# Performance work log

Measured on AMD Instinct MI355X. Metric: run time of the kernel, lower is better.

Reference implementation:

```python
import jax, jax.numpy as jnp
import numpy as np

B, L, D_IN, D_OUT = 8, 2048, 256, 256


def setup_inputs() -> dict:
    key = jax.random.key(0)
    ks = jax.random.split(key, 7)
    s_in = 1.0 / np.sqrt(D_IN)
    return {
        "x": jax.random.normal(ks[0], (B, L, D_IN), dtype=jnp.float32),
        "Wq": jax.random.uniform(ks[1], (D_OUT, D_IN), jnp.float32, -s_in, s_in),
        "bq": jax.random.uniform(ks[2], (D_OUT,), jnp.float32, -s_in, s_in),
        "Wk": jax.random.uniform(ks[3], (D_OUT, D_IN), jnp.float32, -s_in, s_in),
        "bk": jax.random.uniform(ks[4], (D_OUT,), jnp.float32, -s_in, s_in),
        "Wv": jax.random.uniform(ks[5], (D_OUT, D_IN), jnp.float32, -s_in, s_in),
        "bv": jax.random.uniform(ks[6], (D_OUT,), jnp.float32, -s_in, s_in),
    }


def reference(x, Wq, bq, Wk, bk, Wv, bv):
    # QKV projections (torch Linear: y = x @ W.T + b)
    Q = jnp.einsum("bld,od->blo", x, Wq) + bq  # [B, L, D_OUT]
    K = jnp.einsum("bld,od->blo", x, Wk) + bk
    V = jnp.einsum("bld,od->blo", x, Wv) + bv
    scale = jnp.float32(D_OUT) ** 0.5
    E = jnp.einsum("bqd,bkd->bqk", Q, K) / scale  # [B, L, L]
    # NON-STANDARD: softmax over dim=1 (the query axis / columns of E)
    A = jax.nn.softmax(E, axis=1)
    C = jnp.einsum("bqk,bkd->bqd", A, V)  # [B, L, D_OUT]
    S_p = jnp.concatenate([Q, C], axis=1)  # [B, 2L, D_OUT]
    return (S_p, A)
```

## Files before the change

### kernel.cpp

```cpp
#include <hip/hip_runtime.h>
#include <hip/hip_bf16.h>
#include <stdint.h>

#define B_ 8
#define L_ 2048
#define D_ 256

typedef unsigned short u16;
typedef __attribute__((ext_vector_type(4))) float f32x4;
typedef __attribute__((ext_vector_type(8))) short bf16x8;

__device__ __forceinline__ u16 f2b(float f) {
  union { float f; unsigned u; } v; v.f = f;
  unsigned r = v.u + 0x7FFFu + ((v.u >> 16) & 1u);
  return (u16)(r >> 16);
}

__device__ __forceinline__ float b2f(u16 h) {
  union { unsigned u; float f; } v; v.u = (unsigned)h << 16; return v.f;
}

__device__ __forceinline__ void comb(float& m, float& s, float m2, float s2) {
  float mn = fmaxf(m, m2);
  s = s * __expf(m - mn) + s2 * __expf(m2 - mn);
  m = mn;
}

__device__ __forceinline__ void async_copy16(const void* g, u16* l) {
  __builtin_amdgcn_global_load_lds(
      (const __attribute__((address_space(1))) unsigned*)g,
      (__attribute__((address_space(3))) unsigned*)l,
      16, 0, 0);
}

template<int KD>
__device__ __forceinline__ void gemm_core_db(const u16* __restrict__ Ag,
                                             const u16* __restrict__ Bg,
                                             int tile_m, int tile_n,
                                             u16* lds, f32x4 acc[4][4]) {
  const int tid  = threadIdx.x;
  const int wave = tid >> 6, lane = tid & 63;
  const int qd = lane >> 4, ln = lane & 15;
  const int wm = wave >> 1, wn = wave & 1;
  const int lrow = lane >> 2;
  const int lcol = (lane & 3) * 8;
  const u16* Abase = Ag + (size_t)tile_m * KD + lcol;
  const u16* Bbase = Bg + (size_t)tile_n * KD + lcol;
  constexpr int NT = KD / 32;

#pragma unroll
  for (int j = 0; j < 2; ++j) {
    const int r0 = j * 64 + wave * 16;
    async_copy16(Abase + (size_t)(r0 + lrow) * KD, lds + r0 * 32);
    async_copy16(Bbase + (size_t)(r0 + lrow) * KD, lds + 4096 + r0 * 32);
  }

#pragma unroll
  for (int t = 0; t < NT; ++t) {
    asm volatile("s_waitcnt vmcnt(0)" ::: "memory");
    __builtin_amdgcn_s_barrier();
    __builtin_amdgcn_sched_barrier(0);
    const int cur = (t & 1) * 8192;
    if (t + 1 < NT) {
      const int nxt = ((t + 1) & 1) * 8192;
      const int k0 = (t + 1) * 32;
#pragma unroll
      for (int j = 0; j < 2; ++j) {
        const int r0 = j * 64 + wave * 16;
        async_copy16(Abase + (size_t)(r0 + lrow) * KD + k0, lds + nxt + r0 * 32);
        async_copy16(Bbase + (size_t)(r0 + lrow) * KD + k0, lds + nxt + 4096 + r0 * 32);
      }
      __builtin_amdgcn_sched_barrier(0);
    }
    bf16x8 af[4], bg[4];
#pragma unroll
    for (int i = 0; i < 4; ++i) {
      af[i] = *(const bf16x8*)(lds + cur + (wm * 64 + i * 16 + ln) * 32 + qd * 8);
      bg[i] = *(const bf16x8*)(lds + cur + 4096 + (wn * 64 + i * 16 + ln) * 32 + qd * 8);
    }
#pragma unroll
    for (int i = 0; i < 4; ++i)
#pragma unroll
      for (int j = 0; j < 4; ++j)
        acc[i][j] = __builtin_amdgcn_mfma_f32_16x16x32_bf16(af[i], bg[j], acc[i][j], 0, 0, 0);
  }
}

__global__ __launch_bounds__(256) void cvt_kernel(const float* __restrict__ x,
    const float* __restrict__ Wq, const float* __restrict__ Wk, const float* __restrict__ Wv,
    u16* __restrict__ xb, u16* __restrict__ Wb) {
  const int i = blockIdx.x * 256 + threadIdx.x;
  const int NX4 = (B_ * L_ * D_) / 4;
  f32x4 v;
  u16* dst;
  if (i < NX4) {
    v = ((const f32x4*)x)[i];
    dst = xb + (size_t)i * 4;
  } else {
    int wi = i - NX4;
    int z = wi >> 14;
    int off = wi & 16383;
    const float* W = (z == 0) ? Wq : (z == 1 ? Wk : Wv);
    v = ((const f32x4*)W)[off];
    dst = Wb + (size_t)z * 65536 + (size_t)off * 4;
  }
  unsigned p0 = (unsigned)f2b(v.x) | ((unsigned)f2b(v.y) << 16);
  unsigned p1 = (unsigned)f2b(v.z) | ((unsigned)f2b(v.w) << 16);
  *(uint2*)dst = make_uint2(p0, p1);
}

__global__ __launch_bounds__(256) void qkv_gemm(const u16* __restrict__ xb, const u16* __restrict__ Wb,
    const float* __restrict__ bq, const float* __restrict__ bk, const float* __restrict__ bv,
    u16* __restrict__ Qb, u16* __restrict__ Kb, u16* __restrict__ Vbt,
    float* __restrict__ out_sp) {
  __shared__ u16 lds[16384];
  const int z = blockIdx.z;
  const float* bias = (z == 0) ? bq : (z == 1 ? bk : bv);
  const int tile_m = blockIdx.x * 128, tile_n = blockIdx.y * 128;
  f32x4 acc[4][4];
#pragma unroll
  for (int i = 0; i < 4; ++i)
#pragma unroll
    for (int j = 0; j < 4; ++j) acc[i][j] = (f32x4){0.f, 0.f, 0.f, 0.f};
  gemm_core_db<256>(xb, Wb + (size_t)z * 256 * 256, tile_m, tile_n, lds, acc);

  const int tid = threadIdx.x, lane = tid & 63, wave = tid >> 6;
  const int qd = lane >> 4, ln = lane & 15, wm = wave >> 1, wn = wave & 1;

  if (z < 2) {
    u16* dst = (z == 0) ? Qb : Kb;
#pragma unroll
    for (int p = 0; p < 2; ++p) {
      __syncthreads();
      if (wm == p) {
#pragma unroll
        for (int i = 0; i < 4; ++i)
#pragma unroll
          for (int j = 0; j < 4; ++j) {
            const int col = wn * 64 + j * 16 + ln;
            const float bvv = bias[tile_n + col];
#pragma unroll
            for (int r = 0; r < 4; ++r) {
              const int row = i * 16 + qd * 4 + r;
              const float val = acc[i][j][r] + bvv;
              lds[row * 128 + col] = f2b(val);
              if (z == 0) {
                const int grow = tile_m + p * 64 + row;
                const int bb = grow >> 11, l = grow & 2047;
                out_sp[((size_t)bb * (2 * L_) + l) * D_ + tile_n + col] = val;
              }
            }
          }
      }
      __syncthreads();
      const int r = tid >> 2;
#pragma unroll
      for (int s = 0; s < 4; ++s) {
        const int chunk = (tid & 3) + s * 4;
        bf16x8 v = *(const bf16x8*)(lds + r * 128 + chunk * 8);
        *(bf16x8*)(dst + (size_t)(tile_m + p * 64 + r) * D_ + tile_n + chunk * 8) = v;
      }
    }
  } else {
    const int bb = tile_m >> 11, l0 = tile_m & 2047;
    u16* dstb = Vbt + (size_t)bb * D_ * L_;
#pragma unroll
    for (int p = 0; p < 2; ++p) {
      __syncthreads();
      if (wn == p) {
#pragma unroll
        for (int i = 0; i < 4; ++i)
#pragma unroll
          for (int j = 0; j < 4; ++j) {
            const int col = j * 16 + ln;
            const float bvv = bias[tile_n + p * 64 + col];
#pragma unroll
            for (int r = 0; r < 4; ++r) {
              const int row = wm * 64 + i * 16 + qd * 4 + r;
              lds[col * 128 + row] = f2b(acc[i][j][r] + bvv);
            }
          }
      }
      __syncthreads();
      const int dr = tid >> 2;
#pragma unroll
      for (int s = 0; s < 4; ++s) {
        const int chunk = (tid & 3) + s * 4;
        bf16x8 v = *(const bf16x8*)(lds + dr * 128 + chunk * 8);
        *(bf16x8*)(dstb + (size_t)(tile_n + p * 64 + dr) * L_ + l0 + chunk * 8) = v;
      }
    }
  }
}

__global__ __launch_bounds__(256) void e_gemm(const u16* __restrict__ Qb, const u16* __restrict__ Kb,
                                              u16* __restrict__ Eb16,
                                              float* __restrict__ pm, float* __restrict__ ps) {
  __shared__ u16 lds[16384];
  __shared__ float sm_m[4][64], sm_s[4][64];
  const int b = blockIdx.z;
  const int tile_m = blockIdx.x * 128, tile_n = blockIdx.y * 128;
  f32x4 acc[4][4];
#pragma unroll
  for (int i = 0; i < 4; ++i)
#pragma unroll
    for (int j = 0; j < 4; ++j) acc[i][j] = (f32x4){0.f, 0.f, 0.f, 0.f};
  gemm_core_db<256>(Qb + (size_t)b * L_ * D_, Kb + (size_t)b * L_ * D_, tile_m, tile_n, lds, acc);

  u16* Eb = Eb16 + (size_t)b * L_ * L_;
  const int tid = threadIdx.x;
  const int lane = tid & 63, wave = tid >> 6;
  const int qd = lane >> 4, ln = lane & 15, wm = wave >> 1, wn = wave & 1;

#pragma unroll
  for (int j = 0; j < 4; ++j) {
    float m = -1e30f;
#pragma unroll
    for (int i = 0; i < 4; ++i)
#pragma unroll
      for (int r = 0; r < 4; ++r)
        m = fmaxf(m, acc[i][j][r] * 0.0625f);
    float s = 0.f;
#pragma unroll
    for (int i = 0; i < 4; ++i)
#pragma unroll
      for (int r = 0; r < 4; ++r)
        s += __expf(acc[i][j][r] * 0.0625f - m);
    comb(m, s, __shfl_xor(m, 16), __shfl_xor(s, 16));
    comb(m, s, __shfl_xor(m, 32), __shfl_xor(s, 32));
    if (qd == 0) { sm_m[wave][j * 16 + ln] = m; sm_s[wave][j * 16 + ln] = s; }
  }
  __syncthreads();
  if (tid < 128) {
    const int w = tid >> 6, c = tid & 63;
    float m = sm_m[w][c], s = sm_s[w][c];
    comb(m, s, sm_m[w + 2][c], sm_s[w + 2][c]);
    const size_t idx = (size_t)blockIdx.x * (B_ * L_) + (size_t)b * L_ + tile_n + w * 64 + c;
    pm[idx] = m;
    ps[idx] = s;
  }

#pragma unroll
  for (int p = 0; p < 2; ++p) {
    __syncthreads();
    if (wm == p) {
#pragma unroll
      for (int i = 0; i < 4; ++i)
#pragma unroll
        for (int j = 0; j < 4; ++j) {
          const int col = wn * 64 + j * 16 + ln;
#pragma unroll
          for (int r = 0; r < 4; ++r) {
            const int row = i * 16 + qd * 4 + r;
            lds[row * 128 + col] = f2b(acc[i][j][r] * 0.0625f);
          }
        }
    }
    __syncthreads();
    const int r = tid >> 2;
#pragma unroll
    for (int s = 0; s < 4; ++s) {
      const int chunk = (tid & 3) + s * 4;
      bf16x8 v = *(const bf16x8*)(lds + r * 128 + chunk * 8);
      *(bf16x8*)(Eb + (size_t)(tile_m + p * 64 + r) * L_ + tile_n + chunk * 8) = v;
    }
  }
}

__global__ __launch_bounds__(256) void stats_reduce(const float* __restrict__ pm,
                                                    const float* __restrict__ ps,
                                                    float* __restrict__ mOut, float* __restrict__ rOut) {
  const int idx = blockIdx.x * 256 + threadIdx.x;
  float m = -1e30f, s = 0.f;
#pragma unroll
  for (int t = 0; t < 16; ++t)
    comb(m, s, pm[t * (B_ * L_) + idx], ps[t * (B_ * L_) + idx]);
  mOut[idx] = m;
  rOut[idx] = 1.0f / s;
}

__global__ __launch_bounds__(256) void av_fused(const u16* __restrict__ Eb16, const u16* __restrict__ Vbt,
                                                const float* __restrict__ mArr, const float* __restrict__ rArr,
                                                float* __restrict__ Aout, float* __restrict__ out_sp) {
  __shared__ __align__(16) u16 lds_b[2][2][256 * 32];
  __shared__ __align__(16) u16 lds_a[2][2][32 * 32];
  const int b = blockIdx.x;
  const int tile_m = blockIdx.y * 32;
  const int tid = threadIdx.x;
  const int wave = tid >> 6, lane = tid & 63;
  const int qd = lane >> 4, ln = lane & 15;
  const int lrow = lane >> 2, lcol = (lane & 3) * 8;

  const u16* Vb_ = Vbt + (size_t)b * D_ * L_ + lcol;
  const int arow = tid >> 3, koff = (tid & 7) * 8;
  const int aks = koff >> 5, acol = koff & 31;
  const u16* Erow = Eb16 + ((size_t)b * L_ + tile_m + arow) * L_ + koff;
  float* Arow = Aout + ((size_t)b * L_ + tile_m + arow) * L_ + koff;
  const float* mrow = mArr + (size_t)b * L_ + koff;
  const float* rrow = rArr + (size_t)b * L_ + koff;

  f32x4 acc[2][4];
#pragma unroll
  for (int i = 0; i < 2; ++i)
#pragma unroll
    for (int j = 0; j < 4; ++j) acc[i][j] = (f32x4){0.f, 0.f, 0.f, 0.f};

#pragma unroll
  for (int jj = 0; jj < 4; ++jj) {
    const int r0 = wave * 64 + jj * 16;
#pragma unroll
    for (int ks = 0; ks < 2; ++ks)
      async_copy16(Vb_ + (size_t)(r0 + lrow) * L_ + ks * 32, &lds_b[0][ks][r0 * 32]);
  }
  bf16x8 ev = *(const bf16x8*)(Erow);
  f32x4 mv0 = *(const f32x4*)(mrow), mv1 = *(const f32x4*)(mrow + 4);
  f32x4 rv0 = *(const f32x4*)(rrow), rv1 = *(const f32x4*)(rrow + 4);

  for (int t = 0; t < 32; ++t) {
    const int k0 = t * 64;
    const int cur = t & 1;
    float a0 = __expf(b2f((u16)ev[0]) - mv0.x) * rv0.x;
    float a1 = __expf(b2f((u16)ev[1]) - mv0.y) * rv0.y;
    float a2 = __expf(b2f((u16)ev[2]) - mv0.z) * rv0.z;
    float a3 = __expf(b2f((u16)ev[3]) - mv0.w) * rv0.w;
    float a4 = __expf(b2f((u16)ev[4]) - mv1.x) * rv1.x;
    float a5 = __expf(b2f((u16)ev[5]) - mv1.y) * rv1.y;
    float a6 = __expf(b2f((u16)ev[6]) - mv1.z) * rv1.z;
    float a7 = __expf(b2f((u16)ev[7]) - mv1.w) * rv1.w;
    *(f32x4*)(Arow + k0)     = (f32x4){a0, a1, a2, a3};
    *(f32x4*)(Arow + k0 + 4) = (f32x4){a4, a5, a6, a7};
    uint4 pk;
    pk.x = (unsigned)f2b(a0) | ((unsigned)f2b(a1) << 16);
    pk.y = (unsigned)f2b(a2) | ((unsigned)f2b(a3) << 16);
    pk.z = (unsigned)f2b(a4) | ((unsigned)f2b(a5) << 16);
    pk.w = (unsigned)f2b(a6) | ((unsigned)f2b(a7) << 16);
    *(uint4*)(&lds_a[cur][aks][arow * 32 + acol]) = pk;
    const int kn = (k0 + 64) & (L_ - 1);
    ev  = *(const bf16x8*)(Erow + kn);
    mv0 = *(const f32x4*)(mrow + kn);
    mv1 = *(const f32x4*)(mrow + kn + 4);
    rv0 = *(const f32x4*)(rrow + kn);
    rv1 = *(const f32x4*)(rrow + kn + 4);
    asm volatile("s_waitcnt vmcnt(7) lgkmcnt(0)" ::: "memory");
    __builtin_amdgcn_s_barrier();
    __builtin_amdgcn_sched_barrier(0);
    if (t + 1 < 32) {
#pragma unroll
      for (int jj = 0; jj < 4; ++jj) {
        const int r0 = wave * 64 + jj * 16;
#pragma unroll
        for (int ks = 0; ks < 2; ++ks)
          async_copy16(Vb_ + (size_t)(r0 + lrow) * L_ + k0 + 64 + ks * 32,
                       &lds_b[cur ^ 1][ks][r0 * 32]);
      }
      __builtin_amdgcn_sched_barrier(0);
    }
    bf16x8 af[2][2], bg[4][2];
#pragma unroll
    for (int i = 0; i < 2; ++i)
#pragma unroll
      for (int ks = 0; ks < 2; ++ks)
        af[i][ks] = *(const bf16x8*)(&lds_a[cur][ks][(i * 16 + ln) * 32 + qd * 8]);
#pragma unroll
    for (int j = 0; j < 4; ++j)
#pragma unroll
      for (int ks = 0; ks < 2; ++ks)
        bg[j][ks] = *(const bf16x8*)(&lds_b[cur][ks][(wave * 64 + j * 16 + ln) * 32 + qd * 8]);
#pragma unroll
    for (int ks = 0; ks < 2; ++ks)
#pragma unroll
      for (int i = 0; i < 2; ++i)
#pragma unroll
        for (int j = 0; j < 4; ++j)
          acc[i][j] = __builtin_amdgcn_mfma_f32_16x16x32_bf16(af[i][ks], bg[j][ks], acc[i][j], 0, 0, 0);
  }

#pragma unroll
  for (int i = 0; i < 2; ++i)
#pragma unroll
    for (int j = 0; j < 4; ++j) {
      const int col = wave * 64 + j * 16 + ln;
      const int row0 = tile_m + i * 16 + qd * 4;
#pragma unroll
      for (int r = 0; r < 4; ++r)
        out_sp[((size_t)b * (2 * L_) + L_ + row0 + r) * D_ + col] = acc[i][j][r];
    }
}

extern "C" void kernel_launch(void* const* d_in, const int* in_sizes, int n_in,
                              void* d_out, int out_size, void* d_ws, size_t ws_size,
                              hipStream_t stream) {
  const float* x  = (const float*)d_in[0];
  const float* Wq = (const float*)d_in[1];
  const float* bq = (const float*)d_in[2];
  const float* Wk = (const float*)d_in[3];
  const float* bk = (const float*)d_in[4];
  const float* Wv = (const float*)d_in[5];
  const float* bv = (const float*)d_in[6];

  float* out    = (float*)d_out;
  float* outA   = out + (size_t)B_ * (2 * L_) * D_;

  u16* w    = (u16*)d_ws;
  u16* xb   = w;
  u16* Wb   = xb + 4194304;
  u16* Qb   = Wb + 196608;
  u16* Kb   = Qb + 4194304;
  u16* Vbt  = Kb + 4194304;
  u16* Eb16 = Vbt + 4194304;
  float* mArr = (float*)(Eb16 + 33554432);
  float* rArr = mArr + B_ * L_;
  float* pm   = rArr + B_ * L_;
  float* ps   = pm + 16 * B_ * L_;

  cvt_kernel<<<4288, 256, 0, stream>>>(x, Wq, Wk, Wv, xb, Wb);
  qkv_gemm<<<dim3(128, 2, 3), 256, 0, stream>>>(xb, Wb, bq, bk, bv, Qb, Kb, Vbt, out);
  e_gemm<<<dim3(16, 16, 8), 256, 0, stream>>>(Qb, Kb, Eb16, pm, ps);
  stats_reduce<<<64, 256, 0, stream>>>(pm, ps, mArr, rArr);
  av_fused<<<dim3(8, 64), 256, 0, stream>>>(Eb16, Vbt, mArr, rArr, outA, out);
}
```

Measured before the change: 297.3 us.

## Load V fragments directly into registers instead of staging through LDS

The A·V kernel no longer stages V tiles in LDS with async copies. Each lane now loads its MFMA B-operand fragments straight from global memory into registers, double-buffered across two register sets in a two-step unrolled loop. This removes the LDS traffic and most of the LDS footprint for V, which may allow higher occupancy. In exchange it issues strided, less coalesced global loads (each lane reads 16 bytes from a different row) and uses more registers.

Result: slower. 327.9 us (+10.3%).

```diff
diff --git a/kernel.cpp b/kernel.cpp
--- a/kernel.cpp
+++ b/kernel.cpp
@@ -282,16 +282,15 @@
 __global__ __launch_bounds__(256) void av_fused(const u16* __restrict__ Eb16, const u16* __restrict__ Vbt,
                                                 const float* __restrict__ mArr, const float* __restrict__ rArr,
                                                 float* __restrict__ Aout, float* __restrict__ out_sp) {
-  __shared__ __align__(16) u16 lds_b[2][2][256 * 32];
   __shared__ __align__(16) u16 lds_a[2][2][32 * 32];
   const int b = blockIdx.x;
   const int tile_m = blockIdx.y * 32;
   const int tid = threadIdx.x;
   const int wave = tid >> 6, lane = tid & 63;
   const int qd = lane >> 4, ln = lane & 15;
-  const int lrow = lane >> 2, lcol = (lane & 3) * 8;
-
-  const u16* Vb_ = Vbt + (size_t)b * D_ * L_ + lcol;
+
+  const u16* Vfrag = Vbt + (size_t)b * D_ * L_ + (size_t)(wave * 64 + ln) * L_ + qd * 8;
+
   const int arow = tid >> 3, koff = (tid & 7) * 8;
   const int aks = koff >> 5, acol = koff & 31;
   const u16* Erow = Eb16 + ((size_t)b * L_ + tile_m + arow) * L_ + koff;
@@ -305,75 +304,64 @@
 #pragma unroll
     for (int j = 0; j < 4; ++j) acc[i][j] = (f32x4){0.f, 0.f, 0.f, 0.f};
 
-#pragma unroll
-  for (int jj = 0; jj < 4; ++jj) {
-    const int r0 = wave * 64 + jj * 16;
-#pragma unroll
-    for (int ks = 0; ks < 2; ++ks)
-      async_copy16(Vb_ + (size_t)(r0 + lrow) * L_ + ks * 32, &lds_b[0][ks][r0 * 32]);
-  }
   bf16x8 ev = *(const bf16x8*)(Erow);
   f32x4 mv0 = *(const f32x4*)(mrow), mv1 = *(const f32x4*)(mrow + 4);
   f32x4 rv0 = *(const f32x4*)(rrow), rv1 = *(const f32x4*)(rrow + 4);
-
-  for (int t = 0; t < 32; ++t) {
-    const int k0 = t * 64;
-    const int cur = t & 1;
-    float a0 = __expf(b2f((u16)ev[0]) - mv0.x) * rv0.x;
-    float a1 = __expf(b2f((u16)ev[1]) - mv0.y) * rv0.y;
-    float a2 = __expf(b2f((u16)ev[2]) - mv0.z) * rv0.z;
-    float a3 = __expf(b2f((u16)ev[3]) - mv0.w) * rv0.w;
-    float a4 = __expf(b2f((u16)ev[4]) - mv1.x) * rv1.x;
-    float a5 = __expf(b2f((u16)ev[5]) - mv1.y) * rv1.y;
-    float a6 = __expf(b2f((u16)ev[6]) - mv1.z) * rv1.z;
-    float a7 = __expf(b2f((u16)ev[7]) - mv1.w) * rv1.w;
-    *(f32x4*)(Arow + k0)     = (f32x4){a0, a1, a2, a3};
-    *(f32x4*)(Arow + k0 + 4) = (f32x4){a4, a5, a6, a7};
-    uint4 pk;
-    pk.x = (unsigned)f2b(a0) | ((unsigned)f2b(a1) << 16);
-    pk.y = (unsigned)f2b(a2) | ((unsigned)f2b(a3) << 16);
-    pk.z = (unsigned)f2b(a4) | ((unsigned)f2b(a5) << 16);
-    pk.w = (unsigned)f2b(a6) | ((unsigned)f2b(a7) << 16);
-    *(uint4*)(&lds_a[cur][aks][arow * 32 + acol]) = pk;
-    const int kn = (k0 + 64) & (L_ - 1);
-    ev  = *(const bf16x8*)(Erow + kn);
-    mv0 = *(const f32x4*)(mrow + kn);
-    mv1 = *(const f32x4*)(mrow + kn + 4);
-    rv0 = *(const f32x4*)(rrow + kn);
-    rv1 = *(const f32x4*)(rrow + kn + 4);
-    asm volatile("s_waitcnt vmcnt(7) lgkmcnt(0)" ::: "memory");
-    __builtin_amdgcn_s_barrier();
-    __builtin_amdgcn_sched_barrier(0);
-    if (t + 1 < 32) {
-#pragma unroll
-      for (int jj = 0; jj < 4; ++jj) {
-        const int r0 = wave * 64 + jj * 16;
-#pragma unroll
-        for (int ks = 0; ks < 2; ++ks)
-          async_copy16(Vb_ + (size_t)(r0 + lrow) * L_ + k0 + 64 + ks * 32,
-                       &lds_b[cur ^ 1][ks][r0 * 32]);
-      }
-      __builtin_amdgcn_sched_barrier(0);
-    }
-    bf16x8 af[2][2], bg[4][2];
-#pragma unroll
-    for (int i = 0; i < 2; ++i)
-#pragma unroll
-      for (int ks = 0; ks < 2; ++ks)
-        af[i][ks] = *(const bf16x8*)(&lds_a[cur][ks][(i * 16 + ln) * 32 + qd * 8]);
-#pragma unroll
-    for (int j = 0; j < 4; ++j)
-#pragma unroll
-      for (int ks = 0; ks < 2; ++ks)
-        bg[j][ks] = *(const bf16x8*)(&lds_b[cur][ks][(wave * 64 + j * 16 + ln) * 32 + qd * 8]);
+  bf16x8 bgA[4][2], bgB[4][2];
+#pragma unroll
+  for (int j = 0; j < 4; ++j)
 #pragma unroll
     for (int ks = 0; ks < 2; ++ks)
-#pragma unroll
-      for (int i = 0; i < 2; ++i)
-#pragma unroll
-        for (int j = 0; j < 4; ++j)
-          acc[i][j] = __builtin_amdgcn_mfma_f32_16x16x32_bf16(af[i][ks], bg[j][ks], acc[i][j], 0, 0, 0);
-  }
+      bgA[j][ks] = *(const bf16x8*)(Vfrag + (size_t)(j * 16) * L_ + ks * 32);
+
+#define AV_STEP(K0, LBUF, BGC, BGN)                                           \
+  {                                                                           \
+    float a0 = __expf(b2f((u16)ev[0]) - mv0.x) * rv0.x;                       \
+    float a1 = __expf(b2f((u16)ev[1]) - mv0.y) * rv0.y;                       \
+    float a2 = __expf(b2f((u16)ev[2]) - mv0.z) * rv0.z;                       \
+    float a3 = __expf(b2f((u16)ev[3]) - mv0.w) * rv0.w;                       \
+    float a4 = __expf(b2f((u16)ev[4]) - mv1.x) * rv1.x;                       \
+    float a5 = __expf(b2f((u16)ev[5]) - mv1.y) * rv1.y;                       \
+    float a6 = __expf(b2f((u16)ev[6]) - mv1.z) * rv1.z;                       \
+    float a7 = __expf(b2f((u16)ev[7]) - mv1.w) * rv1.w;                       \
+    *(f32x4*)(Arow + (K0))     = (f32x4){a0, a1, a2, a3};                     \
+    *(f32x4*)(Arow + (K0) + 4) = (f32x4){a4, a5, a6, a7};                     \
+    uint4 pk;                                                                 \
+    pk.x = (unsigned)f2b(a0) | ((unsigned)f2b(a1) << 16);                     \
+    pk.y = (unsigned)f2b(a2) | ((unsigned)f2b(a3) << 16);                     \
+    pk.z = (unsigned)f2b(a4) | ((unsigned)f2b(a5) << 16);                     \
+    pk.w = (unsigned)f2b(a6) | ((unsigned)f2b(a7) << 16);                     \
+    *(uint4*)(&lds_a[LBUF][aks][arow * 32 + acol]) = pk;                      \
+    const int kn = ((K0) + 64) & (L_ - 1);                                    \
+    ev  = *(const bf16x8*)(Erow + kn);                                        \
+    mv0 = *(const f32x4*)(mrow + kn); mv1 = *(const f32x4*)(mrow + kn + 4);   \
+    rv0 = *(const f32x4*)(rrow + kn); rv1 = *(const f32x4*)(rrow + kn + 4);   \
+    _Pragma("unroll")                                                         \
+    for (int j = 0; j < 4; ++j)                                               \
+      _Pragma("unroll")                                                       \
+      for (int ks = 0; ks < 2; ++ks)                                          \
+        BGN[j][ks] = *(const bf16x8*)(Vfrag + (size_t)(j * 16) * L_ + kn + ks * 32); \
+    __syncthreads();                                                          \
+    bf16x8 af[2][2];                                                          \
+    _Pragma("unroll")                                                         \
+    for (int i = 0; i < 2; ++i)                                               \
+      _Pragma("unroll")                                                       \
+      for (int ks = 0; ks < 2; ++ks)                                          \
+        af[i][ks] = *(const bf16x8*)(&lds_a[LBUF][ks][(i * 16 + ln) * 32 + qd * 8]); \
+    _Pragma("unroll")                                                         \
+    for (int ks = 0; ks < 2; ++ks)                                            \
+      _Pragma("unroll")                                                       \
+      for (int i = 0; i < 2; ++i)                                             \
+        _Pragma("unroll")                                                     \
+        for (int j = 0; j < 4; ++j)                                           \
+          acc[i][j] = __builtin_amdgcn_mfma_f32_16x16x32_bf16(af[i][ks], BGC[j][ks], acc[i][j], 0, 0, 0); \
+  }
+
+  for (int t = 0; t < 16; ++t) {
+    AV_STEP(t * 128,      0, bgA, bgB)
+    AV_STEP(t * 128 + 64, 1, bgB, bgA)
+  }
+#undef AV_STEP
 
 #pragma unroll
   for (int i = 0; i < 2; ++i)
```
